# Performance work log

Measured on AMD Instinct MI355X. Metric: run time of the kernel, lower is better.

Reference implementation:

```python
import jax, jax.numpy as jnp
import numpy as np

B, L, D_MODEL = 2, 1024, 1024
N_LAYERS = 2
D_INNER = 2 * D_MODEL          # expand = 2
D_STATE = 16
D_CONV = 4
DT_RANK = (D_MODEL + 15) // 16  # ceil(d_model/16) = 64
INIT_SCALE = 0.02


def setup_inputs() -> dict:
    key = jax.random.key(0)
    ks = jax.random.split(key, 8)
    f32 = jnp.float32
    dt_init = float(np.log(np.expm1(0.01)))  # softplus^-1(0.01), standard mamba dt bias init
    return {
        "x": jax.random.normal(ks[0], (B, L, D_MODEL), f32),
        "W_in": jax.random.normal(ks[1], (N_LAYERS, 2 * D_INNER, D_MODEL), f32) * INIT_SCALE,
        "conv_w": jax.random.normal(ks[2], (N_LAYERS, D_INNER, D_CONV), f32) * INIT_SCALE,
        "conv_b": jnp.zeros((N_LAYERS, D_INNER), f32),
        "W_x": jax.random.normal(ks[3], (N_LAYERS, DT_RANK + 2 * D_STATE, D_INNER), f32) * INIT_SCALE,
        "W_dt": jax.random.normal(ks[4], (N_LAYERS, D_INNER, DT_RANK), f32) * INIT_SCALE,
        "b_dt": jnp.full((N_LAYERS, D_INNER), dt_init, f32),
        "A_log": jnp.tile(jnp.log(jnp.arange(1, D_STATE + 1, dtype=f32)), (N_LAYERS, D_INNER, 1)),
        "D": jnp.ones((N_LAYERS, D_INNER), f32),
        "W_out": jax.random.normal(ks[5], (N_LAYERS, D_MODEL, D_INNER), f32) * INIT_SCALE,
    }


def _silu(x):
    return x * jax.nn.sigmoid(x)


def _causal_conv1d(u, w, b):
    # u: [B, L, D_INNER], w: [D_INNER, D_CONV] depthwise, b: [D_INNER]
    ut = jnp.pad(jnp.transpose(u, (0, 2, 1)), ((0, 0), (0, 0), (D_CONV - 1, 0)))
    y = jax.lax.conv_general_dilated(
        ut, w[:, None, :], window_strides=(1,), padding='VALID',
        feature_group_count=D_INNER, dimension_numbers=('NCH', 'OIH', 'NCH'))
    return jnp.transpose(y + b[None, :, None], (0, 2, 1))


def _selective_scan(u, dt, A, Bm, Cm, Dvec):
    # u, dt: [B, L, D_INNER]; A: [D_INNER, N]; Bm, Cm: [B, L, N]; Dvec: [D_INNER]
    dA = jnp.exp(dt[..., None] * A)                        # [B,L,Din,N]
    dBu = dt[..., None] * Bm[:, :, None, :] * u[..., None]  # [B,L,Din,N]

    def step(h, xs):
        dA_t, dBu_t, C_t = xs                              # [B,Din,N],[B,Din,N],[B,N]
        h = dA_t * h + dBu_t
        y = jnp.einsum('bdn,bn->bd', h, C_t)
        return h, y

    h0 = jnp.zeros((u.shape[0], D_INNER, D_STATE), u.dtype)
    _, ys = jax.lax.scan(step, h0, (jnp.swapaxes(dA, 0, 1),
                                    jnp.swapaxes(dBu, 0, 1),
                                    jnp.swapaxes(Cm, 0, 1)))
    return jnp.swapaxes(ys, 0, 1) + u * Dvec               # [B,L,Din]


def _mamba_layer(x, W_in, conv_w, conv_b, W_x, W_dt, b_dt, A_log, Dvec, W_out):
    xz = jnp.einsum('bld,ed->ble', x, W_in)                # [B,L,2*Din]
    u, z = jnp.split(xz, 2, axis=-1)
    u = _silu(_causal_conv1d(u, conv_w, conv_b))
    x_dbl = jnp.einsum('bld,rd->blr', u, W_x)              # [B,L,dt_rank+2N]
    dt, Bm, Cm = jnp.split(x_dbl, [DT_RANK, DT_RANK + D_STATE], axis=-1)
    dt = jax.nn.softplus(jnp.einsum('blr,dr->bld', dt, W_dt) + b_dt)
    A = -jnp.exp(A_log)
    y = _selective_scan(u, dt, A, Bm, Cm, Dvec)
    y = y * _silu(z)
    return jnp.einsum('bld,od->blo', y, W_out)


def reference(x, W_in, conv_w, conv_b, W_x, W_dt, b_dt, A_log, D, W_out):
    residual = x
    h = x
    for i in range(N_LAYERS):
        h = _mamba_layer(h, W_in[i], conv_w[i], conv_b[i], W_x[i],
                         W_dt[i], b_dt[i], A_log[i], D[i], W_out[i])
    return h + residual
```

## Files before the change

### kernel.cpp

```cpp
#include <hip/hip_runtime.h>
#include <hip/hip_bf16.h>
#include <math.h>

#define B_ 2
#define L_ 1024
#define DM 1024
#define DIN 2048
#define DS 16
#define DTR 64
#define CHL 64

typedef __attribute__((ext_vector_type(8))) short bf16x8;
typedef __attribute__((ext_vector_type(8))) unsigned short u16x8;
typedef __attribute__((ext_vector_type(4))) float f32x4;
typedef unsigned short ushort_t;
typedef unsigned int uint_t;

__device__ __forceinline__ float sigmoidf_(float x) { return 1.f / (1.f + __expf(-x)); }
__device__ __forceinline__ ushort_t f2b(float f) {
    uint_t b = __float_as_uint(f);
    return (ushort_t)((b + 0x7FFFu + ((b >> 16) & 1u)) >> 16);
}
__device__ __forceinline__ float b2f(ushort_t u) {
    return __uint_as_float(((uint_t)u) << 16);
}
template<int CTRL>
__device__ __forceinline__ float rradd(float x) {
    int y = __builtin_amdgcn_update_dpp(0, __float_as_int(x), CTRL, 0xf, 0xf, true);
    return x + __int_as_float(y);
}

__global__ __launch_bounds__(256) void f2b_k(const float* __restrict__ in,
                                             ushort_t* __restrict__ out, int n)
{
    int i = blockIdx.x * 256 + threadIdx.x;
    if (i < n) out[i] = f2b(in[i]);
}

template<int EPI>
__global__ __launch_bounds__(256) void mgemm(const ushort_t* __restrict__ A,
    const ushort_t* __restrict__ Bt, float* __restrict__ Cf, ushort_t* __restrict__ Cb,
    const float* __restrict__ bias, const float* __restrict__ res,
    int M, int N, int K, int lda, int ldb)
{
    __shared__ ushort_t sA[128 * 32];
    __shared__ ushort_t sB[128 * 32];
    const int tid = threadIdx.x;
    const int lane = tid & 63, wv = tid >> 6;
    const int wm = wv >> 1, wn = wv & 1;
    const int m0 = blockIdx.y * 128, n0 = blockIdx.x * 128;
    const int sr = tid >> 2;
    const int sc = (tid & 3) * 8;
    f32x4 acc[4][4] = {};

    for (int k0 = 0; k0 < K; k0 += 32) {
#pragma unroll
        for (int j = 0; j < 2; ++j) {
            int ra = sr + j * 64;
            int ga = m0 + ra;
            __builtin_amdgcn_global_load_lds(
                (const uint_t*)(A + (size_t)ga * lda + k0 + sc),
                (uint_t*)(sA + ra * 32 + sc), 16, 0, 0);
            int gb = n0 + ra; if (gb >= N) gb = N - 1;
            __builtin_amdgcn_global_load_lds(
                (const uint_t*)(Bt + (size_t)gb * ldb + k0 + sc),
                (uint_t*)(sB + ra * 32 + sc), 16, 0, 0);
        }
        __syncthreads();
        bf16x8 af[4], bfr[4];
#pragma unroll
        for (int i = 0; i < 4; ++i) {
            af[i]  = *(const bf16x8*)(sA + (wm * 64 + i * 16 + (lane & 15)) * 32 + (lane >> 4) * 8);
            bfr[i] = *(const bf16x8*)(sB + (wn * 64 + i * 16 + (lane & 15)) * 32 + (lane >> 4) * 8);
        }
#pragma unroll
        for (int i = 0; i < 4; ++i)
#pragma unroll
            for (int jj = 0; jj < 4; ++jj)
                acc[i][jj] = __builtin_amdgcn_mfma_f32_16x16x32_bf16(af[i], bfr[jj], acc[i][jj], 0, 0, 0);
        __syncthreads();
    }

    const int cr = (lane >> 4) * 4, cc = lane & 15;
#pragma unroll
    for (int i = 0; i < 4; ++i) {
        int mrow = m0 + wm * 64 + i * 16 + cr;
#pragma unroll
        for (int jj = 0; jj < 4; ++jj) {
            int ncol = n0 + wn * 64 + jj * 16 + cc;
            if (ncol < N) {
#pragma unroll
                for (int r = 0; r < 4; ++r) {
                    float v = acc[i][jj][r];
                    size_t off = (size_t)(mrow + r) * N + ncol;
                    if (EPI == 2) {
                        float s = v + bias[ncol];
                        Cb[off] = f2b((s > 20.f) ? s : log1pf(expf(s)));
                    }
                    else { Cb[off] = f2b(v); }
                }
            }
        }
    }
    (void)Cf; (void)res;
}

__global__ __launch_bounds__(256) void mgemm_sk(const ushort_t* __restrict__ A,
    const ushort_t* __restrict__ Bt, float* __restrict__ P,
    int M, int N, int Kslice, int lda, int ldb)
{
    __shared__ ushort_t sA[128 * 32];
    __shared__ ushort_t sB[128 * 32];
    const int tid = threadIdx.x;
    const int lane = tid & 63, wv = tid >> 6;
    const int wm = wv >> 1, wn = wv & 1;
    const int m0 = blockIdx.y * 128;
    const int kbase = blockIdx.z * Kslice;
    const int sr = tid >> 2;
    const int sc = (tid & 3) * 8;
    f32x4 acc[4][4] = {};

    for (int k0 = kbase; k0 < kbase + Kslice; k0 += 32) {
#pragma unroll
        for (int j = 0; j < 2; ++j) {
            int ra = sr + j * 64;
            __builtin_amdgcn_global_load_lds(
                (const uint_t*)(A + (size_t)(m0 + ra) * lda + k0 + sc),
                (uint_t*)(sA + ra * 32 + sc), 16, 0, 0);
            int gb = ra; if (gb >= N) gb = N - 1;
            __builtin_amdgcn_global_load_lds(
                (const uint_t*)(Bt + (size_t)gb * ldb + k0 + sc),
                (uint_t*)(sB + ra * 32 + sc), 16, 0, 0);
        }
        __syncthreads();
        bf16x8 af[4], bfr[4];
#pragma unroll
        for (int i = 0; i < 4; ++i) {
            af[i]  = *(const bf16x8*)(sA + (wm * 64 + i * 16 + (lane & 15)) * 32 + (lane >> 4) * 8);
            bfr[i] = *(const bf16x8*)(sB + (wn * 64 + i * 16 + (lane & 15)) * 32 + (lane >> 4) * 8);
        }
#pragma unroll
        for (int i = 0; i < 4; ++i)
#pragma unroll
            for (int jj = 0; jj < 4; ++jj)
                acc[i][jj] = __builtin_amdgcn_mfma_f32_16x16x32_bf16(af[i], bfr[jj], acc[i][jj], 0, 0, 0);
        __syncthreads();
    }

    const int cr = (lane >> 4) * 4, cc = lane & 15;
    float* Pz = P + (size_t)blockIdx.z * M * 96;
#pragma unroll
    for (int i = 0; i < 4; ++i) {
        int mrow = m0 + wm * 64 + i * 16 + cr;
#pragma unroll
        for (int jj = 0; jj < 4; ++jj) {
            int ncol = wn * 64 + jj * 16 + cc;
            if (ncol < 96) {
#pragma unroll
                for (int r = 0; r < 4; ++r)
                    Pz[(size_t)(mrow + r) * 96 + ncol] = acc[i][jj][r];
            }
        }
    }
}

__global__ __launch_bounds__(256) void wxred_k(const float* __restrict__ P,
    float* __restrict__ xdbl, ushort_t* __restrict__ xdblb)
{
    int idx = blockIdx.x * 256 + threadIdx.x;
    float s = 0.f;
#pragma unroll
    for (int z = 0; z < 8; ++z) s += P[(size_t)z * 196608 + idx];
    xdbl[idx] = s;
    xdblb[idx] = f2b(s);
}

template<int EPI>
__global__ __launch_bounds__(256) void mgemm_n64(const ushort_t* __restrict__ A,
    const ushort_t* __restrict__ Bt, float* __restrict__ Cf, ushort_t* __restrict__ Cb,
    const float* __restrict__ res, int M, int N, int K, int lda, int ldb)
{
    __shared__ ushort_t sA[128 * 32];
    __shared__ ushort_t sB[64 * 32];
    const int tid = threadIdx.x;
    const int lane = tid & 63, wv = tid >> 6;
    const int m0 = blockIdx.y * 128, n0 = blockIdx.x * 64;
    const int sr = tid >> 2;
    const int sc = (tid & 3) * 8;
    f32x4 acc[2][4] = {};

    for (int k0 = 0; k0 < K; k0 += 32) {
#pragma unroll
        for (int j = 0; j < 2; ++j) {
            int ra = sr + j * 64;
            __builtin_amdgcn_global_load_lds(
                (const uint_t*)(A + (size_t)(m0 + ra) * lda + k0 + sc),
                (uint_t*)(sA + ra * 32 + sc), 16, 0, 0);
        }
        __builtin_amdgcn_global_load_lds(
            (const uint_t*)(Bt + (size_t)(n0 + sr) * ldb + k0 + sc),
            (uint_t*)(sB + sr * 32 + sc), 16, 0, 0);
        __syncthreads();
        bf16x8 af[2], bfr[4];
#pragma unroll
        for (int i = 0; i < 2; ++i)
            af[i]  = *(const bf16x8*)(sA + (wv * 32 + i * 16 + (lane & 15)) * 32 + (lane >> 4) * 8);
#pragma unroll
        for (int jj = 0; jj < 4; ++jj)
            bfr[jj] = *(const bf16x8*)(sB + (jj * 16 + (lane & 15)) * 32 + (lane >> 4) * 8);
#pragma unroll
        for (int i = 0; i < 2; ++i)
#pragma unroll
            for (int jj = 0; jj < 4; ++jj)
                acc[i][jj] = __builtin_amdgcn_mfma_f32_16x16x32_bf16(af[i], bfr[jj], acc[i][jj], 0, 0, 0);
        __syncthreads();
    }

    const int cr = (lane >> 4) * 4, cc = lane & 15;
#pragma unroll
    for (int i = 0; i < 2; ++i) {
        int mrow = m0 + wv * 32 + i * 16 + cr;
#pragma unroll
        for (int jj = 0; jj < 4; ++jj) {
            int ncol = n0 + jj * 16 + cc;
#pragma unroll
            for (int r = 0; r < 4; ++r) {
                float v = acc[i][jj][r];
                size_t off = (size_t)(mrow + r) * N + ncol;
                if (EPI == 3) Cb[off] = f2b(v);
                else Cf[off] = v + res[off];
            }
        }
    }
}

__global__ __launch_bounds__(256) void conv8_k(const ushort_t* __restrict__ xzb,
    const float* __restrict__ cw, const float* __restrict__ cb,
    float* __restrict__ uc, ushort_t* __restrict__ ucb)
{
    int idx8 = blockIdx.x * 256 + threadIdx.x;
    int d8 = (idx8 & 255) * 8;
    int t = (idx8 >> 8) & (L_ - 1);
    int b = idx8 >> 18;
    const ushort_t* base = xzb + (size_t)b * L_ * (2 * DIN) + d8;
    float acc[8];
    const float4* cb4 = (const float4*)(cb + d8);
    float4 cbl = cb4[0], cbh = cb4[1];
#pragma unroll
    for (int e = 0; e < 4; ++e) { acc[e] = ((const float*)&cbl)[e]; acc[4 + e] = ((const float*)&cbh)[e]; }
    float4 cwv[8];
#pragma unroll
    for (int e = 0; e < 8; ++e) cwv[e] = ((const float4*)cw)[d8 + e];
#pragma unroll
    for (int j = 0; j < 4; ++j) {
        int tt = t - 3 + j;
        if (tt >= 0) {
            u16x8 row = *(const u16x8*)(base + (size_t)tt * (2 * DIN));
#pragma unroll
            for (int e = 0; e < 8; ++e)
                acc[e] = fmaf(((const float*)&cwv[e])[j], b2f(row[e]), acc[e]);
        }
    }
    size_t off = (size_t)idx8 * 8;
    u16x8 ob;
#pragma unroll
    for (int e = 0; e < 8; ++e) {
        float v = acc[e] * sigmoidf_(acc[e]);
        uc[off + e] = v;
        ob[e] = f2b(v);
    }
    *(u16x8*)(ucb + off) = ob;
}

__global__ __launch_bounds__(256) void scan_s1(const ushort_t* __restrict__ dtfb,
    const float* __restrict__ uc, const float* __restrict__ xdbl,
    const float* __restrict__ A_log,
    float* __restrict__ bnd_q, float* __restrict__ bnd_s)
{
    __shared__ uint_t sdtp[CHL * 16];
    __shared__ float sB[CHL * 16];
    const int tid = threadIdx.x;
    const int g = tid >> 4, n = tid & 15;
    const int bx = blockIdx.x;
    const int c = bx & 15;
    const int dgrp = (bx >> 4) & 127;
    const int b = bx >> 11;
    const int dbase = dgrp << 4;
    const int t0 = c * CHL;
    const float A_dn = -__expf(A_log[(size_t)(dbase + g) * DS + n]);

#pragma unroll
    for (int k = 0; k < 4; ++k) {
        int idx = tid + k * 256; int i = idx >> 4, jj = idx & 15;
        size_t off = (size_t)(b * L_ + t0 + i) * DIN + dbase + jj;
        ushort_t dtb = dtfb[off];
        float uv = uc[off];
        sdtp[idx] = (uint_t)dtb | ((uint_t)f2b(b2f(dtb) * uv) << 16);
        sB[idx] = xdbl[(size_t)(b * L_ + t0 + i) * 96 + 64 + jj];
    }
    __syncthreads();
    float q = 0.f, s = 0.f;
#pragma unroll 8
    for (int i = 0; i < CHL; ++i) {
        uint_t dp = sdtp[i * 16 + g];
        float dtv = __uint_as_float(dp << 16);
        float dtu = __uint_as_float(dp & 0xffff0000u);
        float Bv  = sB[i * 16 + n];
        float dA  = __expf(dtv * A_dn);
        q = fmaf(dA, q, dtu * Bv);
        s += dtv;
    }
    bnd_q[(size_t)bx * 256 + tid] = q;
    if (n == 0) bnd_s[(size_t)bx * 16 + g] = s;
}

__global__ __launch_bounds__(256) void scan_s2(const ushort_t* __restrict__ dtfb,
    const float* __restrict__ uc, const float* __restrict__ xdbl,
    const ushort_t* __restrict__ xzb, const float* __restrict__ A_log,
    const float* __restrict__ Dvec, const float* __restrict__ bnd_q,
    const float* __restrict__ bnd_s, ushort_t* __restrict__ ucb)
{
    __shared__ float sBCi[CHL * 32];
    __shared__ uint_t sdtp[CHL * 16];
    __shared__ float suT[16 * 65];
    __shared__ float sy3[CHL * 17];
    __shared__ float sD[16];
    const int tid = threadIdx.x;
    const int g = tid >> 4, n = tid & 15;
    const int bx = blockIdx.x;
    const int c = bx & 15;
    const int dgrp = (bx >> 4) & 127;
    const int b = bx >> 11;
    const int dbase = dgrp << 4;
    const int t0 = c * CHL;
    const float A_dn = -__expf(A_log[(size_t)(dbase + g) * DS + n]);
    if (tid < 16) sD[tid] = Dvec[dbase + tid];

#pragma unroll
    for (int j = 0; j < 4; ++j) {
        int idx = tid + j * 256; int i = idx >> 4, jj = idx & 15;
        size_t row = (size_t)(b * L_ + t0 + i);
        sBCi[i * 32 + jj * 2]     = xdbl[row * 96 + 64 + jj];
        sBCi[i * 32 + jj * 2 + 1] = xdbl[row * 96 + 80 + jj];
        size_t off = row * DIN + dbase + jj;
        ushort_t dtb = dtfb[off];
        float uv = uc[off];
        sdtp[idx] = (uint_t)dtb | ((uint_t)f2b(b2f(dtb) * uv) << 16);
        suT[jj * 65 + i] = uv;
    }

    float hs = 0.f;
    const size_t base_bx = (size_t)(b * 2048 + dgrp * 16);
    for (int cc = 0; cc < c; ++cc) {
        float qv = bnd_q[(base_bx + cc) * 256 + tid];
        float sv = bnd_s[(base_bx + cc) * 16 + g];
        hs = fmaf(__expf(A_dn * sv), hs, qv);
    }
    __syncthreads();

#pragma unroll 8
    for (int i = 0; i < CHL; ++i) {
        uint_t dp = sdtp[i * 16 + g];
        float dtv = __uint_as_float(dp << 16);
        float dtu = __uint_as_float(dp & 0xffff0000u);
        float2 bc = *(const float2*)(sBCi + i * 32 + n * 2);
        float dA  = __expf(dtv * A_dn);
        hs = fmaf(dA, hs, dtu * bc.x);
        float p = hs * bc.y;
        p = rradd<0x128>(p);
        p = rradd<0x124>(p);
        p = rradd<0x122>(p);
        p = rradd<0x121>(p);
        if (n == 0) sy3[i * 17 + g] = p;
    }
    __syncthreads();
#pragma unroll
    for (int k = 0; k < 4; ++k) {
        int idx = tid + k * 256; int row = idx >> 4, col = idx & 15;
        float y = sy3[row * 17 + col] + suT[col * 65 + row] * sD[col];
        float z = b2f(xzb[(size_t)(b * L_ + t0 + row) * (2 * DIN) + DIN + dbase + col]);
        y *= z * sigmoidf_(z);
        ucb[(size_t)(b * L_ + t0 + row) * DIN + dbase + col] = f2b(y);
    }
}

extern "C" void kernel_launch(void* const* d_in, const int* in_sizes, int n_in,
                              void* d_out, int out_size, void* d_ws, size_t ws_size,
                              hipStream_t stream)
{
    (void)in_sizes; (void)n_in; (void)out_size; (void)ws_size;
    const float* x      = (const float*)d_in[0];
    const float* W_in   = (const float*)d_in[1];
    const float* conv_w = (const float*)d_in[2];
    const float* conv_b = (const float*)d_in[3];
    const float* W_x    = (const float*)d_in[4];
    const float* W_dt   = (const float*)d_in[5];
    const float* b_dt   = (const float*)d_in[6];
    const float* A_log  = (const float*)d_in[7];
    const float* Dv     = (const float*)d_in[8];
    const float* W_out  = (const float*)d_in[9];
    float* out = (float*)d_out;

    float* uc      = (float*)d_ws;
    float* xdbl    = uc + 4194304;
    float* bnd_q   = xdbl + 196608;
    float* bnd_s   = bnd_q + 1048576;
    float* pws     = bnd_q;
    float* f32_end = bnd_q + 1572864;
    ushort_t* dtfb = (ushort_t*)f32_end;
    ushort_t* xzb  = dtfb + 4194304;
    ushort_t* ucb  = xzb + 8388608;
    ushort_t* xdblb= ucb + 4194304;
    ushort_t* xb   = xdblb + 196608;
    ushort_t* wib  = xb + 2097152;
    ushort_t* wxb  = wib + 8388608;
    ushort_t* wdb  = wxb + 393216;
    ushort_t* wob  = wdb + 262144;

    const int M = B_ * L_;
    f2b_k<<<2097152 / 256, 256, 0, stream>>>(x, xb, 2097152);
    f2b_k<<<8388608 / 256, 256, 0, stream>>>(W_in, wib, 8388608);
    f2b_k<<<(393216 + 255) / 256, 256, 0, stream>>>(W_x, wxb, 393216);
    f2b_k<<<(262144 + 255) / 256, 256, 0, stream>>>(W_dt, wdb, 262144);
    f2b_k<<<4194304 / 256, 256, 0, stream>>>(W_out, wob, 4194304);

    for (int layer = 0; layer < 2; ++layer) {
        mgemm<3><<<dim3(4096 / 128, M / 128), 256, 0, stream>>>(
            xb, wib + (size_t)layer * 4194304, nullptr, xzb, nullptr, nullptr,
            M, 2 * DIN, DM, DM, DM);
        conv8_k<<<(B_ * L_ * DIN / 8) / 256, 256, 0, stream>>>(
            xzb, conv_w + (size_t)layer * DIN * 4, conv_b + (size_t)layer * DIN, uc, ucb);
        mgemm_sk<<<dim3(1, M / 128, 8), 256, 0, stream>>>(
            ucb, wxb + (size_t)layer * 196608, pws, M, 96, DIN / 8, DIN, DIN);
        wxred_k<<<196608 / 256, 256, 0, stream>>>(pws, xdbl, xdblb);
        mgemm<2><<<dim3(2048 / 128, M / 128), 256, 0, stream>>>(
            xdblb, wdb + (size_t)layer * 131072, nullptr, dtfb,
            b_dt + (size_t)layer * DIN, nullptr, M, DIN, DTR, 96, DTR);
        scan_s1<<<4096, 256, 0, stream>>>(dtfb, uc, xdbl,
            A_log + (size_t)layer * DIN * DS, bnd_q, bnd_s);
        scan_s2<<<4096, 256, 0, stream>>>(dtfb, uc, xdbl, xzb,
            A_log + (size_t)layer * DIN * DS, Dv + (size_t)layer * DIN,
            bnd_q, bnd_s, ucb);
        if (layer == 0)
            mgemm_n64<3><<<dim3(1024 / 64, M / 128), 256, 0, stream>>>(
                ucb, wob + (size_t)layer * 2097152, nullptr, xb, nullptr,
                M, DM, DIN, DIN, DIN);
        else
            mgemm_n64<4><<<dim3(1024 / 64, M / 128), 256, 0, stream>>>(
                ucb, wob + (size_t)layer * 2097152, out, nullptr, x,
                M, DM, DIN, DIN, DIN);
    }
}
```

Before: 494.6 us.

## Restructure selective scan to thread-per-channel with separate carry pass; fuse conversions, swizzle GEMMs

The chunked scan now gives each thread one channel with all 16 states in registers, uses 32 chunks of 32 steps, and adds a separate kernel that propagates chunk boundary states in one sequential pass. This replaces the previous quadratic per-chunk carry loop and the cross-lane DPP reductions. The fp32 copy of the conv output is dropped, so the scan reads the bf16 u directly. The five bf16 conversion launches are merged into one, and GEMM tiles get an XCD-aware block swizzle. Costs are more registers per thread and reduced precision for u in the scan. scan_s2 reads ucb as input and writes its output to the same buffer. Each thread only touches its own channel column, so this in-place update looks safe.

```diff
diff --git a/kernel.cpp b/kernel.cpp
--- a/kernel.cpp
+++ b/kernel.cpp
@@ -8,7 +8,8 @@
 #define DIN 2048
 #define DS 16
 #define DTR 64
-#define CHL 64
+#define CHL 32
+#define NCH 32
 
 typedef __attribute__((ext_vector_type(8))) short bf16x8;
 typedef __attribute__((ext_vector_type(8))) unsigned short u16x8;
@@ -24,31 +25,43 @@
 __device__ __forceinline__ float b2f(ushort_t u) {
     return __uint_as_float(((uint_t)u) << 16);
 }
-template<int CTRL>
-__device__ __forceinline__ float rradd(float x) {
-    int y = __builtin_amdgcn_update_dpp(0, __float_as_int(x), CTRL, 0xf, 0xf, true);
-    return x + __int_as_float(y);
-}
-
-__global__ __launch_bounds__(256) void f2b_k(const float* __restrict__ in,
-                                             ushort_t* __restrict__ out, int n)
+
+__global__ __launch_bounds__(256) void f2b_all_k(
+    const float* __restrict__ s0, ushort_t* __restrict__ d0, int n0,
+    const float* __restrict__ s1, ushort_t* __restrict__ d1, int n1,
+    const float* __restrict__ s2, ushort_t* __restrict__ d2, int n2,
+    const float* __restrict__ s3, ushort_t* __restrict__ d3, int n3,
+    const float* __restrict__ s4, ushort_t* __restrict__ d4, int n4)
 {
     int i = blockIdx.x * 256 + threadIdx.x;
-    if (i < n) out[i] = f2b(in[i]);
+    if (i < n0) d0[i] = f2b(s0[i]);
+    i -= n0;
+    if (i >= 0 && i < n1) d1[i] = f2b(s1[i]);
+    i -= n1;
+    if (i >= 0 && i < n2) d2[i] = f2b(s2[i]);
+    i -= n2;
+    if (i >= 0 && i < n3) d3[i] = f2b(s3[i]);
+    i -= n3;
+    if (i >= 0 && i < n4) d4[i] = f2b(s4[i]);
+}
+
+__device__ __forceinline__ int xcd_swz(int wgid, int nwg) {
+    int cpx = nwg >> 3;
+    return (wgid & 7) * cpx + (wgid >> 3);
 }
 
 template<int EPI>
 __global__ __launch_bounds__(256) void mgemm(const ushort_t* __restrict__ A,
     const ushort_t* __restrict__ Bt, float* __restrict__ Cf, ushort_t* __restrict__ Cb,
-    const float* __restrict__ bias, const float* __restrict__ res,
-    int M, int N, int K, int lda, int ldb)
+    const float* __restrict__ bias, int M, int N, int K, int lda, int ldb)
 {
     __shared__ ushort_t sA[128 * 32];
     __shared__ ushort_t sB[128 * 32];
     const int tid = threadIdx.x;
     const int lane = tid & 63, wv = tid >> 6;
     const int wm = wv >> 1, wn = wv & 1;
-    const int m0 = blockIdx.y * 128, n0 = blockIdx.x * 128;
+    const int swz = xcd_swz(blockIdx.y * gridDim.x + blockIdx.x, gridDim.x * gridDim.y);
+    const int m0 = (swz / gridDim.x) * 128, n0 = (swz % gridDim.x) * 128;
     const int sr = tid >> 2;
     const int sc = (tid & 3) * 8;
     f32x4 acc[4][4] = {};
@@ -102,7 +115,7 @@
             }
         }
     }
-    (void)Cf; (void)res;
+    (void)Cf;
 }
 
 __global__ __launch_bounds__(256) void mgemm_sk(const ushort_t* __restrict__ A,
@@ -184,7 +197,8 @@
     __shared__ ushort_t sB[64 * 32];
     const int tid = threadIdx.x;
     const int lane = tid & 63, wv = tid >> 6;
-    const int m0 = blockIdx.y * 128, n0 = blockIdx.x * 64;
+    const int swz = xcd_swz(blockIdx.y * gridDim.x + blockIdx.x, gridDim.x * gridDim.y);
+    const int m0 = (swz / gridDim.x) * 128, n0 = (swz % gridDim.x) * 64;
     const int sr = tid >> 2;
     const int sc = (tid & 3) * 8;
     f32x4 acc[2][4] = {};
@@ -236,7 +250,7 @@
 
 __global__ __launch_bounds__(256) void conv8_k(const ushort_t* __restrict__ xzb,
     const float* __restrict__ cw, const float* __restrict__ cb,
-    float* __restrict__ uc, ushort_t* __restrict__ ucb)
+    ushort_t* __restrict__ ucb)
 {
     int idx8 = blockIdx.x * 256 + threadIdx.x;
     int d8 = (idx8 & 255) * 8;
@@ -261,126 +275,148 @@
                 acc[e] = fmaf(((const float*)&cwv[e])[j], b2f(row[e]), acc[e]);
         }
     }
-    size_t off = (size_t)idx8 * 8;
     u16x8 ob;
 #pragma unroll
     for (int e = 0; e < 8; ++e) {
         float v = acc[e] * sigmoidf_(acc[e]);
-        uc[off + e] = v;
         ob[e] = f2b(v);
     }
-    *(u16x8*)(ucb + off) = ob;
-}
-
-__global__ __launch_bounds__(256) void scan_s1(const ushort_t* __restrict__ dtfb,
-    const float* __restrict__ uc, const float* __restrict__ xdbl,
+    *(u16x8*)(ucb + (size_t)idx8 * 8) = ob;
+}
+
+__global__ __launch_bounds__(256, 2) void scan_s1(const ushort_t* __restrict__ dtfb,
+    const ushort_t* __restrict__ ucb, const float* __restrict__ xdbl,
     const float* __restrict__ A_log,
     float* __restrict__ bnd_q, float* __restrict__ bnd_s)
 {
-    __shared__ uint_t sdtp[CHL * 16];
+    __shared__ uint_t sdt[CHL * 256];
     __shared__ float sB[CHL * 16];
     const int tid = threadIdx.x;
-    const int g = tid >> 4, n = tid & 15;
     const int bx = blockIdx.x;
-    const int c = bx & 15;
-    const int dgrp = (bx >> 4) & 127;
-    const int b = bx >> 11;
-    const int dbase = dgrp << 4;
-    const int t0 = c * CHL;
-    const float A_dn = -__expf(A_log[(size_t)(dbase + g) * DS + n]);
-
-#pragma unroll
-    for (int k = 0; k < 4; ++k) {
-        int idx = tid + k * 256; int i = idx >> 4, jj = idx & 15;
-        size_t off = (size_t)(b * L_ + t0 + i) * DIN + dbase + jj;
-        ushort_t dtb = dtfb[off];
-        float uv = uc[off];
-        sdtp[idx] = (uint_t)dtb | ((uint_t)f2b(b2f(dtb) * uv) << 16);
-        sB[idx] = xdbl[(size_t)(b * L_ + t0 + i) * 96 + 64 + jj];
+    const int dg = bx & 7, c = (bx >> 3) & 31, b = bx >> 8;
+    const int d = dg * 256 + tid;
+    const int row0 = b * L_ + c * CHL;
+
+    float A_dn[16];
+#pragma unroll
+    for (int n = 0; n < 16; ++n) A_dn[n] = -__expf(A_log[(size_t)d * DS + n]);
+
+    for (int k = 0; k < CHL; ++k) {
+        size_t off = (size_t)(row0 + k) * DIN + d;
+        sdt[k * 256 + tid] = (uint_t)dtfb[off] | ((uint_t)ucb[off] << 16);
+    }
+#pragma unroll
+    for (int j = 0; j < 2; ++j) {
+        int idx = tid + j * 256;
+        int t = idx >> 4, n = idx & 15;
+        sB[idx] = xdbl[(size_t)(row0 + t) * 96 + 64 + n];
     }
     __syncthreads();
-    float q = 0.f, s = 0.f;
-#pragma unroll 8
-    for (int i = 0; i < CHL; ++i) {
-        uint_t dp = sdtp[i * 16 + g];
-        float dtv = __uint_as_float(dp << 16);
-        float dtu = __uint_as_float(dp & 0xffff0000u);
-        float Bv  = sB[i * 16 + n];
-        float dA  = __expf(dtv * A_dn);
-        q = fmaf(dA, q, dtu * Bv);
+
+    float q[16];
+#pragma unroll
+    for (int n = 0; n < 16; ++n) q[n] = 0.f;
+    float s = 0.f;
+    for (int k = 0; k < CHL; ++k) {
+        uint_t pk = sdt[k * 256 + tid];
+        float dtv = __uint_as_float(pk << 16);
+        float uv  = __uint_as_float(pk & 0xffff0000u);
+        float dtu = dtv * uv;
         s += dtv;
-    }
-    bnd_q[(size_t)bx * 256 + tid] = q;
-    if (n == 0) bnd_s[(size_t)bx * 16 + g] = s;
-}
-
-__global__ __launch_bounds__(256) void scan_s2(const ushort_t* __restrict__ dtfb,
-    const float* __restrict__ uc, const float* __restrict__ xdbl,
+        f32x4 Bq[4];
+#pragma unroll
+        for (int j = 0; j < 4; ++j) Bq[j] = *(const f32x4*)(sB + k * 16 + j * 4);
+#pragma unroll
+        for (int n = 0; n < 16; ++n)
+            q[n] = fmaf(__expf(dtv * A_dn[n]), q[n], dtu * Bq[n >> 2][n & 3]);
+    }
+    float* qp = bnd_q + ((size_t)(b * NCH + c) * DIN + d) * 16;
+#pragma unroll
+    for (int j = 0; j < 4; ++j)
+        *(f32x4*)(qp + j * 4) = (f32x4){q[j * 4], q[j * 4 + 1], q[j * 4 + 2], q[j * 4 + 3]};
+    bnd_s[(size_t)(b * NCH + c) * DIN + d] = s;
+}
+
+__global__ __launch_bounds__(256) void scan_b2(const float* __restrict__ bnd_q,
+    const float* __restrict__ bnd_s, const float* __restrict__ A_log,
+    float* __restrict__ Hini)
+{
+    int glob = blockIdx.x * 256 + threadIdx.x;
+    int n = glob & 15, d = (glob >> 4) & (DIN - 1), b = glob >> 15;
+    float A_dn = -__expf(A_log[(size_t)d * DS + n]);
+    float H = 0.f;
+    for (int c = 0; c < NCH; ++c) {
+        size_t idx = (size_t)(b * NCH + c) * DIN + d;
+        Hini[idx * 16 + n] = H;
+        H = fmaf(__expf(A_dn * bnd_s[idx]), H, bnd_q[idx * 16 + n]);
+    }
+}
+
+__global__ __launch_bounds__(256, 2) void scan_s2(const ushort_t* __restrict__ dtfb,
+    const ushort_t* __restrict__ ucb_in, const float* __restrict__ xdbl,
     const ushort_t* __restrict__ xzb, const float* __restrict__ A_log,
-    const float* __restrict__ Dvec, const float* __restrict__ bnd_q,
-    const float* __restrict__ bnd_s, ushort_t* __restrict__ ucb)
-{
-    __shared__ float sBCi[CHL * 32];
-    __shared__ uint_t sdtp[CHL * 16];
-    __shared__ float suT[16 * 65];
-    __shared__ float sy3[CHL * 17];
-    __shared__ float sD[16];
+    const float* __restrict__ Dvec, const float* __restrict__ Hini,
+    ushort_t* __restrict__ ucb_out)
+{
+    __shared__ uint_t sdt[CHL * 256];
+    __shared__ float sBC[CHL * 32];
+    __shared__ float sy[CHL * 256];
     const int tid = threadIdx.x;
-    const int g = tid >> 4, n = tid & 15;
     const int bx = blockIdx.x;
-    const int c = bx & 15;
-    const int dgrp = (bx >> 4) & 127;
-    const int b = bx >> 11;
-    const int dbase = dgrp << 4;
-    const int t0 = c * CHL;
-    const float A_dn = -__expf(A_log[(size_t)(dbase + g) * DS + n]);
-    if (tid < 16) sD[tid] = Dvec[dbase + tid];
-
+    const int dg = bx & 7, c = (bx >> 3) & 31, b = bx >> 8;
+    const int d = dg * 256 + tid;
+    const int row0 = b * L_ + c * CHL;
+    const float Dd = Dvec[d];
+
+    float A_dn[16];
+#pragma unroll
+    for (int n = 0; n < 16; ++n) A_dn[n] = -__expf(A_log[(size_t)d * DS + n]);
+
+    for (int k = 0; k < CHL; ++k) {
+        size_t off = (size_t)(row0 + k) * DIN + d;
+        sdt[k * 256 + tid] = (uint_t)dtfb[off] | ((uint_t)ucb_in[off] << 16);
+    }
 #pragma unroll
     for (int j = 0; j < 4; ++j) {
-        int idx = tid + j * 256; int i = idx >> 4, jj = idx & 15;
-        size_t row = (size_t)(b * L_ + t0 + i);
-        sBCi[i * 32 + jj * 2]     = xdbl[row * 96 + 64 + jj];
-        sBCi[i * 32 + jj * 2 + 1] = xdbl[row * 96 + 80 + jj];
-        size_t off = row * DIN + dbase + jj;
-        ushort_t dtb = dtfb[off];
-        float uv = uc[off];
-        sdtp[idx] = (uint_t)dtb | ((uint_t)f2b(b2f(dtb) * uv) << 16);
-        suT[jj * 65 + i] = uv;
-    }
-
-    float hs = 0.f;
-    const size_t base_bx = (size_t)(b * 2048 + dgrp * 16);
-    for (int cc = 0; cc < c; ++cc) {
-        float qv = bnd_q[(base_bx + cc) * 256 + tid];
-        float sv = bnd_s[(base_bx + cc) * 16 + g];
-        hs = fmaf(__expf(A_dn * sv), hs, qv);
+        int idx = tid + j * 256;
+        int t = idx >> 5, jj = idx & 31;
+        sBC[idx] = xdbl[(size_t)(row0 + t) * 96 + 64 + (jj & 1) * 16 + (jj >> 1)];
+    }
+
+    float h[16];
+    const float* hp = Hini + ((size_t)(b * NCH + c) * DIN + d) * 16;
+#pragma unroll
+    for (int j = 0; j < 4; ++j) {
+        f32x4 hv = *(const f32x4*)(hp + j * 4);
+#pragma unroll
+        for (int e = 0; e < 4; ++e) h[j * 4 + e] = hv[e];
     }
     __syncthreads();
 
-#pragma unroll 8
-    for (int i = 0; i < CHL; ++i) {
-        uint_t dp = sdtp[i * 16 + g];
-        float dtv = __uint_as_float(dp << 16);
-        float dtu = __uint_as_float(dp & 0xffff0000u);
-        float2 bc = *(const float2*)(sBCi + i * 32 + n * 2);
-        float dA  = __expf(dtv * A_dn);
-        hs = fmaf(dA, hs, dtu * bc.x);
-        float p = hs * bc.y;
-        p = rradd<0x128>(p);
-        p = rradd<0x124>(p);
-        p = rradd<0x122>(p);
-        p = rradd<0x121>(p);
-        if (n == 0) sy3[i * 17 + g] = p;
+    for (int k = 0; k < CHL; ++k) {
+        uint_t pk = sdt[k * 256 + tid];
+        float dtv = __uint_as_float(pk << 16);
+        float uv  = __uint_as_float(pk & 0xffff0000u);
+        float dtu = dtv * uv;
+        float y = uv * Dd;
+        f32x4 bcq[8];
+#pragma unroll
+        for (int j = 0; j < 8; ++j) bcq[j] = *(const f32x4*)(sBC + k * 32 + j * 4);
+#pragma unroll
+        for (int n = 0; n < 16; ++n) {
+            float Bv = bcq[n >> 1][(n & 1) * 2];
+            float Cv = bcq[n >> 1][(n & 1) * 2 + 1];
+            h[n] = fmaf(__expf(dtv * A_dn[n]), h[n], dtu * Bv);
+            y = fmaf(h[n], Cv, y);
+        }
+        sy[k * 256 + tid] = y;
     }
     __syncthreads();
-#pragma unroll
-    for (int k = 0; k < 4; ++k) {
-        int idx = tid + k * 256; int row = idx >> 4, col = idx & 15;
-        float y = sy3[row * 17 + col] + suT[col * 65 + row] * sD[col];
-        float z = b2f(xzb[(size_t)(b * L_ + t0 + row) * (2 * DIN) + DIN + dbase + col]);
+    for (int k = 0; k < CHL; ++k) {
+        float y = sy[k * 256 + tid];
+        float z = b2f(xzb[(size_t)(row0 + k) * (2 * DIN) + DIN + d]);
         y *= z * sigmoidf_(z);
-        ucb[(size_t)(b * L_ + t0 + row) * DIN + dbase + col] = f2b(y);
+        ucb_out[(size_t)(row0 + k) * DIN + d] = f2b(y);
     }
 }
 
@@ -401,13 +437,12 @@
     const float* W_out  = (const float*)d_in[9];
     float* out = (float*)d_out;
 
-    float* uc      = (float*)d_ws;
-    float* xdbl    = uc + 4194304;
-    float* bnd_q   = xdbl + 196608;
-    float* bnd_s   = bnd_q + 1048576;
-    float* pws     = bnd_q;
-    float* f32_end = bnd_q + 1572864;
-    ushort_t* dtfb = (ushort_t*)f32_end;
+    float* xdbl    = (float*)d_ws;
+    float* pws     = xdbl + 196608;
+    float* bnd_q   = pws + 1572864;
+    float* bnd_s   = bnd_q + 2097152;
+    float* Hini    = bnd_s + 131072;
+    ushort_t* dtfb = (ushort_t*)(Hini + 2097152);
     ushort_t* xzb  = dtfb + 4194304;
     ushort_t* ucb  = xzb + 8388608;
     ushort_t* xdblb= ucb + 4194304;
@@ -418,29 +453,28 @@
     ushort_t* wob  = wdb + 262144;
 
     const int M = B_ * L_;
-    f2b_k<<<2097152 / 256, 256, 0, stream>>>(x, xb, 2097152);
-    f2b_k<<<8388608 / 256, 256, 0, stream>>>(W_in, wib, 8388608);
-    f2b_k<<<(393216 + 255) / 256, 256, 0, stream>>>(W_x, wxb, 393216);
-    f2b_k<<<(262144 + 255) / 256, 256, 0, stream>>>(W_dt, wdb, 262144);
-    f2b_k<<<4194304 / 256, 256, 0, stream>>>(W_out, wob, 4194304);
+    const int NT = 2097152 + 8388608 + 393216 + 262144 + 4194304;
+    f2b_all_k<<<(NT + 255) / 256, 256, 0, stream>>>(
+        x, xb, 2097152, W_in, wib, 8388608, W_x, wxb, 393216,
+        W_dt, wdb, 262144, W_out, wob, 4194304);
 
     for (int layer = 0; layer < 2; ++layer) {
         mgemm<3><<<dim3(4096 / 128, M / 128), 256, 0, stream>>>(
-            xb, wib + (size_t)layer * 4194304, nullptr, xzb, nullptr, nullptr,
+            xb, wib + (size_t)layer * 4194304, nullptr, xzb, nullptr,
             M, 2 * DIN, DM, DM, DM);
         conv8_k<<<(B_ * L_ * DIN / 8) / 256, 256, 0, stream>>>(
-            xzb, conv_w + (size_t)layer * DIN * 4, conv_b + (size_t)layer * DIN, uc, ucb);
+            xzb, conv_w + (size_t)layer * DIN * 4, conv_b + (size_t)layer * DIN, ucb);
         mgemm_sk<<<dim3(1, M / 128, 8), 256, 0, stream>>>(
             ucb, wxb + (size_t)layer * 196608, pws, M, 96, DIN / 8, DIN, DIN);
         wxred_k<<<196608 / 256, 256, 0, stream>>>(pws, xdbl, xdblb);
         mgemm<2><<<dim3(2048 / 128, M / 128), 256, 0, stream>>>(
             xdblb, wdb + (size_t)layer * 131072, nullptr, dtfb,
-            b_dt + (size_t)layer * DIN, nullptr, M, DIN, DTR, 96, DTR);
-        scan_s1<<<4096, 256, 0, stream>>>(dtfb, uc, xdbl,
-            A_log + (size_t)layer * DIN * DS, bnd_q, bnd_s);
-        scan_s2<<<4096, 256, 0, stream>>>(dtfb, uc, xdbl, xzb,
-            A_log + (size_t)layer * DIN * DS, Dv + (size_t)layer * DIN,
-            bnd_q, bnd_s, ucb);
+            b_dt + (size_t)layer * DIN, M, DIN, DTR, 96, DTR);
+        const float* Al = A_log + (size_t)layer * DIN * DS;
+        scan_s1<<<B_ * NCH * 8, 256, 0, stream>>>(dtfb, ucb, xdbl, Al, bnd_q, bnd_s);
+        scan_b2<<<(B_ * DIN * 16) / 256, 256, 0, stream>>>(bnd_q, bnd_s, Al, Hini);
+        scan_s2<<<B_ * NCH * 8, 256, 0, stream>>>(dtfb, ucb, xdbl, xzb, Al,
+            Dv + (size_t)layer * DIN, Hini, ucb);
         if (layer == 0)
             mgemm_n64<3><<<dim3(1024 / 64, M / 128), 256, 0, stream>>>(
                 ucb, wob + (size_t)layer * 2097152, nullptr, xb, nullptr,
```

Measured after the change: 479.4 us. 1.03x faster.
